# Kernel tuning notes

Hardware: AMD Instinct MI355X
Metric: run time of the kernel (lower is better)

The kernel has to match this reference:

```python
import jax, jax.numpy as jnp
import numpy as np

DIM = 1024
NUM_HEADS = 16
HEAD_DIM = DIM // NUM_HEADS
ROPE_BASE = 10000.0


def _rope_cos_sin(seq_len, head_dim):
    inv_freq = 1.0 / (ROPE_BASE ** (jnp.arange(0, head_dim, 2, dtype=jnp.float32) / head_dim))
    t = jnp.arange(seq_len, dtype=jnp.float32)
    freqs = t[:, None] * inv_freq[None, :]            # [S, Dh/2]
    emb = jnp.concatenate([freqs, freqs], axis=-1)    # [S, Dh]
    return jnp.cos(emb), jnp.sin(emb)


def _rotate_half(x):
    half = x.shape[-1] // 2
    return jnp.concatenate([-x[..., half:], x[..., :half]], axis=-1)


def setup_inputs() -> dict:
    key = jax.random.key(0)
    k1, k2, k3 = jax.random.split(key, 3)
    B, S = 2, 2048
    x = jax.random.normal(k1, (B, S, DIM), dtype=jnp.float32)
    w_qkv = jax.random.normal(k2, (3 * DIM, DIM), dtype=jnp.float32) * (DIM ** -0.5)
    w_out = jax.random.normal(k3, (DIM, DIM), dtype=jnp.float32) * (DIM ** -0.5)
    return {"x": x, "w_qkv": w_qkv, "w_out": w_out}


def reference(x, w_qkv, w_out):
    B, S, D = x.shape
    H, Dh = NUM_HEADS, HEAD_DIM
    scale = Dh ** -0.5

    qkv = (x @ w_qkv.T).reshape(B, S, 3, H, Dh)      # [B,S,3,H,Dh]
    qkv = jnp.transpose(qkv, (2, 0, 3, 1, 4))        # [3,B,H,S,Dh]
    q, k, v = qkv[0], qkv[1], qkv[2]

    cos, sin = _rope_cos_sin(S, Dh)                  # [S,Dh]
    cos = cos[None, None, :, :]
    sin = sin[None, None, :, :]
    q = q * cos + _rotate_half(q) * sin
    k = k * cos + _rotate_half(k) * sin

    scores = jnp.einsum('bhqd,bhkd->bhqk', q, k) * scale
    causal_mask = jnp.triu(jnp.ones((S, S), dtype=bool), k=1)
    scores = jnp.where(causal_mask[None, None], -jnp.inf, scores)
    attn = jax.nn.softmax(scores, axis=-1)
    out = jnp.einsum('bhqk,bhkd->bhqd', attn, v)      # [B,H,S,Dh]
    out = jnp.transpose(out, (0, 2, 1, 3)).reshape(B, S, D)
    return out @ w_out.T
```

## Files before the change

### kernel.cpp

```cpp
#include <hip/hip_runtime.h>
#include <stdint.h>

typedef uint16_t u16;
typedef __attribute__((ext_vector_type(8))) short bf16x8;
typedef __attribute__((ext_vector_type(4))) float f32x4;

__device__ inline u16 f2b(float f) {
  uint32_t u = __float_as_uint(f);
  u += 0x7FFF + ((u >> 16) & 1);
  return (u16)(u >> 16);
}
__device__ inline float b2f(u16 h) {
  return __uint_as_float(((uint32_t)h) << 16);
}

__global__ void k_detect(const u16* __restrict__ X, int* __restrict__ flag) {
  __shared__ int cnt;
  const int t = threadIdx.x;
  if (t == 0) cnt = 0;
  __syncthreads();
  float av = fabsf(b2f(X[t * 2]));
  int wild = (av < 1000.0f) ? 0 : 1;
  atomicAdd(&cnt, wild);
  __syncthreads();
  if (t == 0) flag[0] = (cnt > 16) ? 1 : 0;
}

__global__ __launch_bounds__(256) void k_qkv_rope(const void* __restrict__ Xv,
                                                  const void* __restrict__ Wv,
                                                  const int* __restrict__ flag,
                                                  u16* __restrict__ Qo,
                                                  u16* __restrict__ Ko,
                                                  u16* __restrict__ Vo) {
  __shared__ u16 As[64][40];
  __shared__ u16 Bs[3][64][40];
  __shared__ float Cs[64][66];
  const int mode = flag[0];
  const int h = blockIdx.x;
  const int n0h = h * 64;
  const int m0 = blockIdx.y * 64;
  const int t = threadIdx.x, w = t >> 6, lane = t & 63;
  const int lr = lane & 15, lq = lane >> 4;
  f32x4 acc[3][4] = {};
  const int rA = t >> 2, cA = (t & 3) * 8;
  const int aoff = (m0 + rA) * 1024 + cA;
  const int boff0 = (n0h + rA) * 1024 + cA;
  for (int k0 = 0; k0 < 1024; k0 += 32) {
    __syncthreads();
    if (mode == 0) {
      *(uint4*)&As[rA][cA]    = *(const uint4*)((const u16*)Xv + aoff + k0);
      *(uint4*)&Bs[0][rA][cA] = *(const uint4*)((const u16*)Wv + boff0 + k0);
      *(uint4*)&Bs[1][rA][cA] = *(const uint4*)((const u16*)Wv + boff0 + 1048576 + k0);
      *(uint4*)&Bs[2][rA][cA] = *(const uint4*)((const u16*)Wv + boff0 + 2097152 + k0);
    } else {
      const float* Xf = (const float*)Xv;
      const float* Wf = (const float*)Wv;
#pragma unroll
      for (int ee = 0; ee < 8; ++ee) {
        As[rA][cA + ee]    = f2b(Xf[aoff + k0 + ee]);
        Bs[0][rA][cA + ee] = f2b(Wf[boff0 + k0 + ee]);
        Bs[1][rA][cA + ee] = f2b(Wf[boff0 + 1048576 + k0 + ee]);
        Bs[2][rA][cA + ee] = f2b(Wf[boff0 + 2097152 + k0 + ee]);
      }
    }
    __syncthreads();
    bf16x8 bf[3];
#pragma unroll
    for (int e = 0; e < 3; ++e)
      bf[e] = *(const bf16x8*)&Bs[e][(w << 4) + lr][lq * 8];
#pragma unroll
    for (int mt = 0; mt < 4; ++mt) {
      bf16x8 af = *(const bf16x8*)&As[(mt << 4) + lr][lq * 8];
#pragma unroll
      for (int e = 0; e < 3; ++e)
        acc[e][mt] = __builtin_amdgcn_mfma_f32_16x16x32_bf16(af, bf[e], acc[e][mt], 0, 0, 0);
    }
  }

  for (int e = 0; e < 3; ++e) {
    __syncthreads();
    {
      const int col = (w << 4) + lr;
#pragma unroll
      for (int mt = 0; mt < 4; ++mt)
#pragma unroll
        for (int i = 0; i < 4; ++i)
          Cs[mt * 16 + lq * 4 + i][col] = acc[e][mt][i];
    }
    __syncthreads();
    if (e == 2) {
      const int sx = t & 63, dh0 = (t >> 6) * 16;
      const int m = m0 + sx, b = m >> 11, s = m & 2047;
      const long hb = (long)(b * 16 + h) * 64;
#pragma unroll
      for (int u = 0; u < 16; ++u) {
        int dh = dh0 + u;
        Vo[(hb + dh) * 2048 + s] = f2b(Cs[sx][dh]);
      }
    } else {
      const int r = t >> 2, dh0 = (t & 3) * 16;
      const int m = m0 + r, b = m >> 11, s = m & 2047;
      const int obase = ((b * 16 + h) * 2048 + s) * 64;
      u16* O = (e == 0) ? Qo : Ko;
#pragma unroll
      for (int u = 0; u < 16; ++u) {
        int dh = dh0 + u;
        float v  = Cs[r][dh];
        float vp = Cs[r][dh ^ 32];
        float sign = (dh < 32) ? -1.0f : 1.0f;
        float fr  = __expf((float)(dh & 31) * -0.28782314f);
        float ang = (float)s * fr;
        float sn = __sinf(ang), cs = __cosf(ang);
        O[obase + dh] = f2b(v * cs + sign * vp * sn);
      }
    }
  }
}

__global__ __launch_bounds__(256) void k_attn(const u16* __restrict__ Q,
                                              const u16* __restrict__ K,
                                              const u16* __restrict__ V,
                                              u16* __restrict__ AO) {
  __shared__ u16 QP[64][72];
  __shared__ u16 Ks[64][72];
  __shared__ u16 Vt[64][72];
  const int qt = 31 - blockIdx.x;
  const int bh = blockIdx.y;
  const int b = bh >> 4, h = bh & 15;
  const u16* Qg = Q + (bh * 2048 + qt * 64) * 64;
  const u16* Kg = K + bh * 2048 * 64;
  const u16* Vg = V + (long)bh * 64 * 2048;
  const int t = threadIdx.x, w = t >> 6, lane = t & 63;
  const int lr = lane & 15, lq = lane >> 4;
  const int lq4 = lq * 4;
  const int base16 = lane & 48;
  const int r0 = t >> 3, c0 = (t & 7) * 8;

  *(uint4*)&QP[r0][c0]      = *(const uint4*)&Qg[r0 * 64 + c0];
  *(uint4*)&QP[r0 + 32][c0] = *(const uint4*)&Qg[(r0 + 32) * 64 + c0];
  __syncthreads();
  bf16x8 qf[2];
#pragma unroll
  for (int kk = 0; kk < 2; ++kk)
    qf[kk] = *(const bf16x8*)&QP[w * 16 + lr][kk * 32 + lq * 8];

  float m_i = -3.0e4f, l_i = 0.f;
  f32x4 o_acc[4] = {};
  const int qrow_l = w * 16 + lr;

  for (int kt = 0; kt <= qt; ++kt) {
    __syncthreads();
    *(uint4*)&Ks[r0][c0]      = *(const uint4*)&Kg[(kt * 64 + r0) * 64 + c0];
    *(uint4*)&Ks[r0 + 32][c0] = *(const uint4*)&Kg[(kt * 64 + r0 + 32) * 64 + c0];
    *(uint4*)&Vt[r0][c0]      = *(const uint4*)&Vg[r0 * 2048 + kt * 64 + c0];
    *(uint4*)&Vt[r0 + 32][c0] = *(const uint4*)&Vg[(r0 + 32) * 2048 + kt * 64 + c0];
    __syncthreads();

    f32x4 sa[4] = {};
#pragma unroll
    for (int mb = 0; mb < 4; ++mb)
#pragma unroll
      for (int kk = 0; kk < 2; ++kk) {
        bf16x8 kf = *(const bf16x8*)&Ks[mb * 16 + lr][kk * 32 + lq * 8];
        sa[mb] = __builtin_amdgcn_mfma_f32_16x16x32_bf16(kf, qf[kk], sa[mb], 0, 0, 0);
      }

    float sc[4][4];
    float m_new = m_i;
#pragma unroll
    for (int mb = 0; mb < 4; ++mb)
#pragma unroll
      for (int i = 0; i < 4; ++i) {
        float sv = sa[mb][i] * 0.125f;
        if (kt == qt && (mb * 16 + lq4 + i) > qrow_l) sv = -3.0e4f;
        sc[mb][i] = sv;
        m_new = fmaxf(m_new, sv);
      }
    m_new = fmaxf(m_new, __shfl_xor(m_new, 16));
    m_new = fmaxf(m_new, __shfl_xor(m_new, 32));
    float alpha = __expf(m_i - m_new);
    m_i = m_new;
    float p[4][4], sm = 0.f;
#pragma unroll
    for (int mb = 0; mb < 4; ++mb)
#pragma unroll
      for (int i = 0; i < 4; ++i) { p[mb][i] = __expf(sc[mb][i] - m_new); sm += p[mb][i]; }
    sm += __shfl_xor(sm, 16);
    sm += __shfl_xor(sm, 32);
    l_i = l_i * alpha + sm;

#pragma unroll
    for (int mb = 0; mb < 4; ++mb) {
      uint2 pk;
      pk.x = (uint32_t)f2b(p[mb][0]) | ((uint32_t)f2b(p[mb][1]) << 16);
      pk.y = (uint32_t)f2b(p[mb][2]) | ((uint32_t)f2b(p[mb][3]) << 16);
      *(uint2*)&QP[w * 16 + lr][mb * 16 + lq4] = pk;
    }

#pragma unroll
    for (int i = 0; i < 4; ++i) {
      float ai = __shfl(alpha, base16 | (lq4 + i));
      o_acc[0][i] *= ai; o_acc[1][i] *= ai;
      o_acc[2][i] *= ai; o_acc[3][i] *= ai;
    }

    asm volatile("s_waitcnt lgkmcnt(0)" ::: "memory");

#pragma unroll
    for (int kk = 0; kk < 2; ++kk) {
      bf16x8 pf = *(const bf16x8*)&QP[w * 16 + lr][kk * 32 + lq * 8];
#pragma unroll
      for (int nb = 0; nb < 4; ++nb) {
        bf16x8 vf = *(const bf16x8*)&Vt[nb * 16 + lr][kk * 32 + lq * 8];
        o_acc[nb] = __builtin_amdgcn_mfma_f32_16x16x32_bf16(pf, vf, o_acc[nb], 0, 0, 0);
      }
    }
  }
  float linv = 1.0f / l_i;
#pragma unroll
  for (int i = 0; i < 4; ++i) {
    float inv = __shfl(linv, base16 | (lq4 + i));
    int row = qt * 64 + w * 16 + lq4 + i;
    int ob = (b * 2048 + row) * 1024 + h * 64;
#pragma unroll
    for (int nb = 0; nb < 4; ++nb)
      AO[ob + nb * 16 + lr] = f2b(o_acc[nb][i] * inv);
  }
}

__global__ __launch_bounds__(256) void k_gemm_out(const u16* __restrict__ A,
                                                  const void* __restrict__ Bv,
                                                  const int* __restrict__ flag,
                                                  void* __restrict__ Cv) {
  __shared__ u16 As[64][40];
  __shared__ u16 Bs[64][40];
  const int mode = flag[0];
  const int n0 = blockIdx.x * 64, m0 = blockIdx.y * 64;
  const int t = threadIdx.x, w = t >> 6, lane = t & 63;
  const int lr = lane & 15, lq = lane >> 4;
  f32x4 acc[4] = {};
  const int rA = t >> 2, cA = (t & 3) * 8;
  const int aoff = (m0 + rA) * 1024 + cA;
  const int boff = (n0 + rA) * 1024 + cA;
  for (int k0 = 0; k0 < 1024; k0 += 32) {
    __syncthreads();
    *(uint4*)&As[rA][cA] = *(const uint4*)(A + aoff + k0);
    if (mode == 0) {
      *(uint4*)&Bs[rA][cA] = *(const uint4*)((const u16*)Bv + boff + k0);
    } else {
      const float* Bf = (const float*)Bv;
#pragma unroll
      for (int e = 0; e < 8; ++e) Bs[rA][cA + e] = f2b(Bf[boff + k0 + e]);
    }
    __syncthreads();
    bf16x8 bf = *(const bf16x8*)&Bs[(w << 4) + lr][lq * 8];
#pragma unroll
    for (int mt = 0; mt < 4; ++mt) {
      bf16x8 af = *(const bf16x8*)&As[(mt << 4) + lr][lq * 8];
      acc[mt] = __builtin_amdgcn_mfma_f32_16x16x32_bf16(af, bf, acc[mt], 0, 0, 0);
    }
  }
  const int col = n0 + (w << 4) + lr;
  if (mode == 0) {
    u16* C = (u16*)Cv;
#pragma unroll
    for (int mt = 0; mt < 4; ++mt)
#pragma unroll
      for (int i = 0; i < 4; ++i)
        C[(m0 + mt * 16 + lq * 4 + i) * 1024 + col] = f2b(acc[mt][i]);
  } else {
    float* C = (float*)Cv;
#pragma unroll
    for (int mt = 0; mt < 4; ++mt)
#pragma unroll
      for (int i = 0; i < 4; ++i)
        C[(m0 + mt * 16 + lq * 4 + i) * 1024 + col] = acc[mt][i];
  }
}

extern "C" void kernel_launch(void* const* d_in, const int* in_sizes, int n_in,
                              void* d_out, int out_size, void* d_ws, size_t ws_size,
                              hipStream_t stream) {
  const void* x    = d_in[0];
  const void* wqkv = d_in[1];
  const void* wout = d_in[2];

  int* flag = (int*)d_ws;
  u16* qb = (u16*)((char*)d_ws + 256);
  u16* kb = qb + 4194304;
  u16* vb = kb + 4194304;
  u16* ao = vb + 4194304;

  k_detect  <<<dim3(1), 256, 0, stream>>>((const u16*)x, flag);
  k_qkv_rope<<<dim3(16, 64), 256, 0, stream>>>(x, wqkv, flag, qb, kb, vb);
  k_attn    <<<dim3(32, 32), 256, 0, stream>>>(qb, kb, vb, ao);
  k_gemm_out<<<dim3(16, 64), 256, 0, stream>>>(ao, wout, flag, d_out);
}
```

Measured before the change: 247.8 us.

## Pair causal query tiles per attention block and widen output GEMM tile

Each attention block now handles two query tiles (qt and 31-qt), sharing the K/V tile loads between them so the causal workload per block is balanced. This halves the grid to 512 blocks and reuses each K/V load across two query tiles. The output projection GEMM now computes a 64x128 tile per block, reusing the A tile across two B tiles and halving that grid. The cost is fewer blocks for latency hiding and more registers per thread. In the attention kernel the P buffer in QP is reused by both tiles, which relies on an LDS wait rather than a barrier between them.

```diff
diff --git a/kernel.cpp b/kernel.cpp
--- a/kernel.cpp
+++ b/kernel.cpp
@@ -76,7 +76,6 @@
         acc[e][mt] = __builtin_amdgcn_mfma_f32_16x16x32_bf16(af, bf[e], acc[e][mt], 0, 0, 0);
     }
   }
-
   for (int e = 0; e < 3; ++e) {
     __syncthreads();
     {
@@ -117,6 +116,68 @@
   }
 }
 
+__device__ __forceinline__ void attn_tile(u16 QP[64][72], u16 Ks[64][72],
+                                          u16 Vt[64][72], const bf16x8 qf[2],
+                                          f32x4 o_acc[4], float& m_i, float& l_i,
+                                          int kt, int qt_tile, int w, int lr,
+                                          int lq, int lq4, int base16, int qrow_l) {
+  f32x4 sa[4] = {};
+#pragma unroll
+  for (int mb = 0; mb < 4; ++mb)
+#pragma unroll
+    for (int kk = 0; kk < 2; ++kk) {
+      bf16x8 kf = *(const bf16x8*)&Ks[mb * 16 + lr][kk * 32 + lq * 8];
+      sa[mb] = __builtin_amdgcn_mfma_f32_16x16x32_bf16(kf, qf[kk], sa[mb], 0, 0, 0);
+    }
+  float sc[4][4];
+  float m_new = m_i;
+#pragma unroll
+  for (int mb = 0; mb < 4; ++mb)
+#pragma unroll
+    for (int i = 0; i < 4; ++i) {
+      float sv = sa[mb][i] * 0.125f;
+      if (kt == qt_tile && (mb * 16 + lq4 + i) > qrow_l) sv = -3.0e4f;
+      sc[mb][i] = sv;
+      m_new = fmaxf(m_new, sv);
+    }
+  m_new = fmaxf(m_new, __shfl_xor(m_new, 16));
+  m_new = fmaxf(m_new, __shfl_xor(m_new, 32));
+  float alpha = __expf(m_i - m_new);
+  m_i = m_new;
+  float p[4][4], sm = 0.f;
+#pragma unroll
+  for (int mb = 0; mb < 4; ++mb)
+#pragma unroll
+    for (int i = 0; i < 4; ++i) { p[mb][i] = __expf(sc[mb][i] - m_new); sm += p[mb][i]; }
+  sm += __shfl_xor(sm, 16);
+  sm += __shfl_xor(sm, 32);
+  l_i = l_i * alpha + sm;
+
+#pragma unroll
+  for (int mb = 0; mb < 4; ++mb) {
+    uint2 pk;
+    pk.x = (uint32_t)f2b(p[mb][0]) | ((uint32_t)f2b(p[mb][1]) << 16);
+    pk.y = (uint32_t)f2b(p[mb][2]) | ((uint32_t)f2b(p[mb][3]) << 16);
+    *(uint2*)&QP[w * 16 + lr][mb * 16 + lq4] = pk;
+  }
+#pragma unroll
+  for (int i = 0; i < 4; ++i) {
+    float ai = __shfl(alpha, base16 | (lq4 + i));
+    o_acc[0][i] *= ai; o_acc[1][i] *= ai;
+    o_acc[2][i] *= ai; o_acc[3][i] *= ai;
+  }
+  asm volatile("s_waitcnt lgkmcnt(0)" ::: "memory");
+#pragma unroll
+  for (int kk = 0; kk < 2; ++kk) {
+    bf16x8 pf = *(const bf16x8*)&QP[w * 16 + lr][kk * 32 + lq * 8];
+#pragma unroll
+    for (int nb = 0; nb < 4; ++nb) {
+      bf16x8 vf = *(const bf16x8*)&Vt[nb * 16 + lr][kk * 32 + lq * 8];
+      o_acc[nb] = __builtin_amdgcn_mfma_f32_16x16x32_bf16(pf, vf, o_acc[nb], 0, 0, 0);
+    }
+  }
+}
+
 __global__ __launch_bounds__(256) void k_attn(const u16* __restrict__ Q,
                                               const u16* __restrict__ K,
                                               const u16* __restrict__ V,
@@ -124,10 +185,11 @@
   __shared__ u16 QP[64][72];
   __shared__ u16 Ks[64][72];
   __shared__ u16 Vt[64][72];
-  const int qt = 31 - blockIdx.x;
+  const int qtA = 31 - blockIdx.x;
+  const int qtB = blockIdx.x;
   const int bh = blockIdx.y;
   const int b = bh >> 4, h = bh & 15;
-  const u16* Qg = Q + (bh * 2048 + qt * 64) * 64;
+  const u16* Qg = Q + (bh * 2048) * 64;
   const u16* Kg = K + bh * 2048 * 64;
   const u16* Vg = V + (long)bh * 64 * 2048;
   const int t = threadIdx.x, w = t >> 6, lane = t & 63;
@@ -135,20 +197,27 @@
   const int lq4 = lq * 4;
   const int base16 = lane & 48;
   const int r0 = t >> 3, c0 = (t & 7) * 8;
-
-  *(uint4*)&QP[r0][c0]      = *(const uint4*)&Qg[r0 * 64 + c0];
-  *(uint4*)&QP[r0 + 32][c0] = *(const uint4*)&Qg[(r0 + 32) * 64 + c0];
-  __syncthreads();
-  bf16x8 qf[2];
+  const int qrow_l = w * 16 + lr;
+
+  bf16x8 qfA[2], qfB[2];
+  *(uint4*)&QP[r0][c0]      = *(const uint4*)&Qg[(qtA * 64 + r0) * 64 + c0];
+  *(uint4*)&QP[r0 + 32][c0] = *(const uint4*)&Qg[(qtA * 64 + r0 + 32) * 64 + c0];
+  __syncthreads();
 #pragma unroll
   for (int kk = 0; kk < 2; ++kk)
-    qf[kk] = *(const bf16x8*)&QP[w * 16 + lr][kk * 32 + lq * 8];
-
-  float m_i = -3.0e4f, l_i = 0.f;
-  f32x4 o_acc[4] = {};
-  const int qrow_l = w * 16 + lr;
-
-  for (int kt = 0; kt <= qt; ++kt) {
+    qfA[kk] = *(const bf16x8*)&QP[w * 16 + lr][kk * 32 + lq * 8];
+  __syncthreads();
+  *(uint4*)&QP[r0][c0]      = *(const uint4*)&Qg[(qtB * 64 + r0) * 64 + c0];
+  *(uint4*)&QP[r0 + 32][c0] = *(const uint4*)&Qg[(qtB * 64 + r0 + 32) * 64 + c0];
+  __syncthreads();
+#pragma unroll
+  for (int kk = 0; kk < 2; ++kk)
+    qfB[kk] = *(const bf16x8*)&QP[w * 16 + lr][kk * 32 + lq * 8];
+
+  float m_iA = -3.0e4f, l_iA = 0.f, m_iB = -3.0e4f, l_iB = 0.f;
+  f32x4 o_accA[4] = {}, o_accB[4] = {};
+
+  for (int kt = 0; kt <= qtA; ++kt) {
     __syncthreads();
     *(uint4*)&Ks[r0][c0]      = *(const uint4*)&Kg[(kt * 64 + r0) * 64 + c0];
     *(uint4*)&Ks[r0 + 32][c0] = *(const uint4*)&Kg[(kt * 64 + r0 + 32) * 64 + c0];
@@ -156,75 +225,28 @@
     *(uint4*)&Vt[r0 + 32][c0] = *(const uint4*)&Vg[(r0 + 32) * 2048 + kt * 64 + c0];
     __syncthreads();
 
-    f32x4 sa[4] = {};
-#pragma unroll
-    for (int mb = 0; mb < 4; ++mb)
-#pragma unroll
-      for (int kk = 0; kk < 2; ++kk) {
-        bf16x8 kf = *(const bf16x8*)&Ks[mb * 16 + lr][kk * 32 + lq * 8];
-        sa[mb] = __builtin_amdgcn_mfma_f32_16x16x32_bf16(kf, qf[kk], sa[mb], 0, 0, 0);
-      }
-
-    float sc[4][4];
-    float m_new = m_i;
-#pragma unroll
-    for (int mb = 0; mb < 4; ++mb)
-#pragma unroll
-      for (int i = 0; i < 4; ++i) {
-        float sv = sa[mb][i] * 0.125f;
-        if (kt == qt && (mb * 16 + lq4 + i) > qrow_l) sv = -3.0e4f;
-        sc[mb][i] = sv;
-        m_new = fmaxf(m_new, sv);
-      }
-    m_new = fmaxf(m_new, __shfl_xor(m_new, 16));
-    m_new = fmaxf(m_new, __shfl_xor(m_new, 32));
-    float alpha = __expf(m_i - m_new);
-    m_i = m_new;
-    float p[4][4], sm = 0.f;
-#pragma unroll
-    for (int mb = 0; mb < 4; ++mb)
-#pragma unroll
-      for (int i = 0; i < 4; ++i) { p[mb][i] = __expf(sc[mb][i] - m_new); sm += p[mb][i]; }
-    sm += __shfl_xor(sm, 16);
-    sm += __shfl_xor(sm, 32);
-    l_i = l_i * alpha + sm;
-
-#pragma unroll
-    for (int mb = 0; mb < 4; ++mb) {
-      uint2 pk;
-      pk.x = (uint32_t)f2b(p[mb][0]) | ((uint32_t)f2b(p[mb][1]) << 16);
-      pk.y = (uint32_t)f2b(p[mb][2]) | ((uint32_t)f2b(p[mb][3]) << 16);
-      *(uint2*)&QP[w * 16 + lr][mb * 16 + lq4] = pk;
-    }
-
-#pragma unroll
-    for (int i = 0; i < 4; ++i) {
-      float ai = __shfl(alpha, base16 | (lq4 + i));
-      o_acc[0][i] *= ai; o_acc[1][i] *= ai;
-      o_acc[2][i] *= ai; o_acc[3][i] *= ai;
-    }
-
-    asm volatile("s_waitcnt lgkmcnt(0)" ::: "memory");
-
-#pragma unroll
-    for (int kk = 0; kk < 2; ++kk) {
-      bf16x8 pf = *(const bf16x8*)&QP[w * 16 + lr][kk * 32 + lq * 8];
-#pragma unroll
-      for (int nb = 0; nb < 4; ++nb) {
-        bf16x8 vf = *(const bf16x8*)&Vt[nb * 16 + lr][kk * 32 + lq * 8];
-        o_acc[nb] = __builtin_amdgcn_mfma_f32_16x16x32_bf16(pf, vf, o_acc[nb], 0, 0, 0);
-      }
-    }
-  }
-  float linv = 1.0f / l_i;
+    attn_tile(QP, Ks, Vt, qfA, o_accA, m_iA, l_iA, kt, qtA,
+              w, lr, lq, lq4, base16, qrow_l);
+    if (kt <= qtB) {
+      asm volatile("s_waitcnt lgkmcnt(0)" ::: "memory");
+      attn_tile(QP, Ks, Vt, qfB, o_accB, m_iB, l_iB, kt, qtB,
+                w, lr, lq, lq4, base16, qrow_l);
+    }
+  }
+  float linvA = 1.0f / l_iA, linvB = 1.0f / l_iB;
 #pragma unroll
   for (int i = 0; i < 4; ++i) {
-    float inv = __shfl(linv, base16 | (lq4 + i));
-    int row = qt * 64 + w * 16 + lq4 + i;
-    int ob = (b * 2048 + row) * 1024 + h * 64;
-#pragma unroll
-    for (int nb = 0; nb < 4; ++nb)
-      AO[ob + nb * 16 + lr] = f2b(o_acc[nb][i] * inv);
+    float invA = __shfl(linvA, base16 | (lq4 + i));
+    float invB = __shfl(linvB, base16 | (lq4 + i));
+    int rowA = qtA * 64 + w * 16 + lq4 + i;
+    int rowB = qtB * 64 + w * 16 + lq4 + i;
+    int obA = (b * 2048 + rowA) * 1024 + h * 64;
+    int obB = (b * 2048 + rowB) * 1024 + h * 64;
+#pragma unroll
+    for (int nb = 0; nb < 4; ++nb) {
+      AO[obA + nb * 16 + lr] = f2b(o_accA[nb][i] * invA);
+      AO[obB + nb * 16 + lr] = f2b(o_accB[nb][i] * invB);
+    }
   }
 }
 
@@ -233,12 +255,12 @@
                                                   const int* __restrict__ flag,
                                                   void* __restrict__ Cv) {
   __shared__ u16 As[64][40];
-  __shared__ u16 Bs[64][40];
+  __shared__ u16 Bs[2][64][40];
   const int mode = flag[0];
-  const int n0 = blockIdx.x * 64, m0 = blockIdx.y * 64;
+  const int n0 = blockIdx.x * 128, m0 = blockIdx.y * 64;
   const int t = threadIdx.x, w = t >> 6, lane = t & 63;
   const int lr = lane & 15, lq = lane >> 4;
-  f32x4 acc[4] = {};
+  f32x4 acc[2][4] = {};
   const int rA = t >> 2, cA = (t & 3) * 8;
   const int aoff = (m0 + rA) * 1024 + cA;
   const int boff = (n0 + rA) * 1024 + cA;
@@ -246,35 +268,47 @@
     __syncthreads();
     *(uint4*)&As[rA][cA] = *(const uint4*)(A + aoff + k0);
     if (mode == 0) {
-      *(uint4*)&Bs[rA][cA] = *(const uint4*)((const u16*)Bv + boff + k0);
+      *(uint4*)&Bs[0][rA][cA] = *(const uint4*)((const u16*)Bv + boff + k0);
+      *(uint4*)&Bs[1][rA][cA] = *(const uint4*)((const u16*)Bv + boff + 65536 + k0);
     } else {
       const float* Bf = (const float*)Bv;
 #pragma unroll
-      for (int e = 0; e < 8; ++e) Bs[rA][cA + e] = f2b(Bf[boff + k0 + e]);
-    }
-    __syncthreads();
-    bf16x8 bf = *(const bf16x8*)&Bs[(w << 4) + lr][lq * 8];
+      for (int e = 0; e < 8; ++e) {
+        Bs[0][rA][cA + e] = f2b(Bf[boff + k0 + e]);
+        Bs[1][rA][cA + e] = f2b(Bf[boff + 65536 + k0 + e]);
+      }
+    }
+    __syncthreads();
+    bf16x8 bfx[2];
+#pragma unroll
+    for (int e = 0; e < 2; ++e)
+      bfx[e] = *(const bf16x8*)&Bs[e][(w << 4) + lr][lq * 8];
 #pragma unroll
     for (int mt = 0; mt < 4; ++mt) {
       bf16x8 af = *(const bf16x8*)&As[(mt << 4) + lr][lq * 8];
-      acc[mt] = __builtin_amdgcn_mfma_f32_16x16x32_bf16(af, bf, acc[mt], 0, 0, 0);
-    }
-  }
-  const int col = n0 + (w << 4) + lr;
-  if (mode == 0) {
-    u16* C = (u16*)Cv;
-#pragma unroll
-    for (int mt = 0; mt < 4; ++mt)
-#pragma unroll
-      for (int i = 0; i < 4; ++i)
-        C[(m0 + mt * 16 + lq * 4 + i) * 1024 + col] = f2b(acc[mt][i]);
-  } else {
-    float* C = (float*)Cv;
-#pragma unroll
-    for (int mt = 0; mt < 4; ++mt)
-#pragma unroll
-      for (int i = 0; i < 4; ++i)
-        C[(m0 + mt * 16 + lq * 4 + i) * 1024 + col] = acc[mt][i];
+#pragma unroll
+      for (int e = 0; e < 2; ++e)
+        acc[e][mt] = __builtin_amdgcn_mfma_f32_16x16x32_bf16(af, bfx[e], acc[e][mt], 0, 0, 0);
+    }
+  }
+#pragma unroll
+  for (int e = 0; e < 2; ++e) {
+    const int col = n0 + e * 64 + (w << 4) + lr;
+    if (mode == 0) {
+      u16* C = (u16*)Cv;
+#pragma unroll
+      for (int mt = 0; mt < 4; ++mt)
+#pragma unroll
+        for (int i = 0; i < 4; ++i)
+          C[(m0 + mt * 16 + lq * 4 + i) * 1024 + col] = f2b(acc[e][mt][i]);
+    } else {
+      float* C = (float*)Cv;
+#pragma unroll
+      for (int mt = 0; mt < 4; ++mt)
+#pragma unroll
+        for (int i = 0; i < 4; ++i)
+          C[(m0 + mt * 16 + lq * 4 + i) * 1024 + col] = acc[e][mt][i];
+    }
   }
 }
 
@@ -293,6 +327,6 @@
 
   k_detect  <<<dim3(1), 256, 0, stream>>>((const u16*)x, flag);
   k_qkv_rope<<<dim3(16, 64), 256, 0, stream>>>(x, wqkv, flag, qb, kb, vb);
-  k_attn    <<<dim3(32, 32), 256, 0, stream>>>(qb, kb, vb, ao);
-  k_gemm_out<<<dim3(16, 64), 256, 0, stream>>>(ao, wout, flag, d_out);
-}
+  k_attn    <<<dim3(16, 32), 256, 0, stream>>>(qb, kb, vb, ao);
+  k_gemm_out<<<dim3(8, 64), 256, 0, stream>>>(ao, wout, flag, d_out);
+}
```

New measurement: 235.6 us. -4.9%, faster.
